# Kernel tuning notes

Hardware: AMD Instinct MI355X
Metric: run time of the kernel (lower is better)

## Reference

```python
import jax, jax.numpy as jnp
import numpy as np

M = 512          # n_clusters
D_PER = 32       # examples per cluster
FEAT = 1024      # embedding dim
ALPHA = 1.0
N_CLASSES = 128
EPS = 1e-8


def setup_inputs() -> dict:
    key = jax.random.key(0)
    k1, k2 = jax.random.split(key)
    N = M * D_PER
    inp = jax.random.normal(k1, (N, FEAT), dtype=jnp.float32)
    # class label per cluster, repeated d times so each contiguous chunk shares a class
    cluster_classes = jax.random.randint(k2, (M,), 0, N_CLASSES, dtype=jnp.int32)
    target = jnp.repeat(cluster_classes, D_PER)
    return {"input": inp, "target": target}


def reference(input, target):
    N, feat = input.shape
    m, d = M, D_PER
    # cluster assignment: sorted arange(m) repeated d times == repeat(arange(m), d)
    clusters = jnp.repeat(jnp.arange(m), d)                      # [N]
    cluster_classes = target[0 : m * d : d]                      # [m]

    # segment mean over contiguous equal-size chunks (== torch.chunk + mean + stack)
    means = input.reshape(m, d, feat).mean(axis=1)               # [m, feat]

    r2 = jnp.sum(input * input, axis=1, keepdims=True)           # [N,1]
    c2 = jnp.sum(means * means, axis=1)                          # [m]
    sample_costs = r2 + c2[None, :] - 2.0 * (input @ means.T)    # [N, m]

    # distance of each example to its own cluster mean
    intra = jnp.take_along_axis(sample_costs, clusters[:, None], axis=1)[:, 0]  # [N]

    variance = jnp.sum(intra) / float(N - 1)
    var_norm = -1.0 / (2.0 * variance ** 2)

    numerator = jnp.exp(var_norm * intra - ALPHA)                # [N]

    diff_class_mask = (target[:, None] != cluster_classes[None, :]).astype(input.dtype)  # [N,m]
    denominator = jnp.sum(diff_class_mask * jnp.exp(var_norm * sample_costs), axis=1)    # [N]

    losses = jax.nn.relu(-jnp.log(numerator / (denominator + EPS) + EPS))
    total_loss = jnp.mean(losses)

    pred = jnp.argmin(sample_costs, axis=1)                      # [N]
    acc = jnp.mean((pred == clusters).astype(jnp.float32))
    return total_loss, losses, pred, acc
```

## Files before the change

### kernel.cpp

```cpp
#include <hip/hip_runtime.h>
#include <math.h>

#define NCLUST 512
#define DPER 32
#define NFEAT 1024
#define NSAMP (NCLUST * DPER)
#define ALPHA_C 1.0f
#define EPS_C 1e-8f
#define MARGIN_C 0.25f

#define GBM 128
#define GBN 128
#define GBK 32
#define NCHUNK 8

typedef __attribute__((ext_vector_type(4))) float f32x4;
typedef __attribute__((ext_vector_type(8))) _Float16 f16x8;

__device__ __forceinline__ unsigned f2h(float f) {
  _Float16 h = (_Float16)f;
  return (unsigned)__builtin_bit_cast(ushort, h);
}

__device__ __forceinline__ void gload16(const ushort* g, ushort* l) {
  __builtin_amdgcn_global_load_lds(
      (const __attribute__((address_space(1))) unsigned int*)g,
      (__attribute__((address_space(3))) unsigned int*)l, 16, 0, 0);
}

__global__ __launch_bounds__(256) void k_pre(const float* __restrict__ inp,
                                             const int* __restrict__ target,
                                             float* __restrict__ means,
                                             ushort* __restrict__ Bf16,
                                             ushort* __restrict__ Af16,
                                             float* __restrict__ c2,
                                             float* __restrict__ r2g,
                                             float* __restrict__ intra,
                                             float* __restrict__ percl,
                                             int* __restrict__ ccls,
                                             int* __restrict__ wcount) {
  const int m = blockIdx.x;
  const int t = threadIdx.x;
  const int w = t >> 6, l = t & 63;
  __shared__ float ldsm[4][NFEAT];
  __shared__ float meanf[NFEAT];
  __shared__ float red4[4];
  __shared__ float redi[4];
  __shared__ float c2sh;

  const float* rowbase = inp + (size_t)m * DPER * NFEAT;
  ushort* arowbase = Af16 + (size_t)m * DPER * NFEAT;

  float4 macc0 = {0,0,0,0}, macc1 = {0,0,0,0}, macc2 = {0,0,0,0}, macc3 = {0,0,0,0};
  float r2keep[8];

  #pragma unroll 2
  for (int rr = 0; rr < 8; ++rr) {
    const int d = w * 8 + rr;
    const float* rp = rowbase + (size_t)d * NFEAT + l * 4;
    const float4 v0 = *(const float4*)(rp);
    const float4 v1 = *(const float4*)(rp + 256);
    const float4 v2 = *(const float4*)(rp + 512);
    const float4 v3 = *(const float4*)(rp + 768);
    ushort* ap = arowbase + (size_t)d * NFEAT + l * 4;
    uint2 h;
    h.x = f2h(v0.x) | (f2h(v0.y) << 16); h.y = f2h(v0.z) | (f2h(v0.w) << 16);
    *(uint2*)(ap) = h;
    h.x = f2h(v1.x) | (f2h(v1.y) << 16); h.y = f2h(v1.z) | (f2h(v1.w) << 16);
    *(uint2*)(ap + 256) = h;
    h.x = f2h(v2.x) | (f2h(v2.y) << 16); h.y = f2h(v2.z) | (f2h(v2.w) << 16);
    *(uint2*)(ap + 512) = h;
    h.x = f2h(v3.x) | (f2h(v3.y) << 16); h.y = f2h(v3.z) | (f2h(v3.w) << 16);
    *(uint2*)(ap + 768) = h;
    macc0.x += v0.x; macc0.y += v0.y; macc0.z += v0.z; macc0.w += v0.w;
    macc1.x += v1.x; macc1.y += v1.y; macc1.z += v1.z; macc1.w += v1.w;
    macc2.x += v2.x; macc2.y += v2.y; macc2.z += v2.z; macc2.w += v2.w;
    macc3.x += v3.x; macc3.y += v3.y; macc3.z += v3.z; macc3.w += v3.w;
    float p = v0.x*v0.x + v0.y*v0.y + v0.z*v0.z + v0.w*v0.w
            + v1.x*v1.x + v1.y*v1.y + v1.z*v1.z + v1.w*v1.w
            + v2.x*v2.x + v2.y*v2.y + v2.z*v2.z + v2.w*v2.w
            + v3.x*v3.x + v3.y*v3.y + v3.z*v3.z + v3.w*v3.w;
    #pragma unroll
    for (int off = 32; off; off >>= 1) p += __shfl_down(p, off);
    r2keep[rr] = p;
  }
  if (l == 0) {
    #pragma unroll
    for (int rr = 0; rr < 8; ++rr) r2g[m * DPER + w * 8 + rr] = r2keep[rr];
  }
  *(float4*)&ldsm[w][0 * 256 + l * 4] = macc0;
  *(float4*)&ldsm[w][1 * 256 + l * 4] = macc1;
  *(float4*)&ldsm[w][2 * 256 + l * 4] = macc2;
  *(float4*)&ldsm[w][3 * 256 + l * 4] = macc3;
  __syncthreads();
  float4 s0 = *(const float4*)&ldsm[0][t * 4];
  float4 s1 = *(const float4*)&ldsm[1][t * 4];
  float4 s2 = *(const float4*)&ldsm[2][t * 4];
  float4 s3 = *(const float4*)&ldsm[3][t * 4];
  const float inv = 1.0f / 32.0f;
  float4 mn;
  mn.x = (s0.x + s1.x + s2.x + s3.x) * inv;
  mn.y = (s0.y + s1.y + s2.y + s3.y) * inv;
  mn.z = (s0.z + s1.z + s2.z + s3.z) * inv;
  mn.w = (s0.w + s1.w + s2.w + s3.w) * inv;
  *(float4*)(means + (size_t)m * NFEAT + t * 4) = mn;
  uint2 bw;
  bw.x = f2h(mn.x) | (f2h(mn.y) << 16);
  bw.y = f2h(mn.z) | (f2h(mn.w) << 16);
  *(uint2*)&Bf16[(size_t)m * NFEAT + t * 4] = bw;
  *(float4*)&meanf[t * 4] = mn;
  float sq = mn.x * mn.x + mn.y * mn.y + mn.z * mn.z + mn.w * mn.w;
  #pragma unroll
  for (int off = 32; off; off >>= 1) sq += __shfl_down(sq, off);
  if (l == 0) red4[w] = sq;
  __syncthreads();
  if (t == 0) {
    const float cc = red4[0] + red4[1] + red4[2] + red4[3];
    c2sh = cc;
    c2[m] = cc;
    ccls[m] = target[m * DPER];
    if (m == 0) *wcount = 0;
  }
  __syncthreads();
  const float c2v = c2sh;
  float sintra = 0.f;
  #pragma unroll 2
  for (int rr = 0; rr < 8; ++rr) {
    const int d = w * 8 + rr;
    const float* rp = rowbase + (size_t)d * NFEAT + l * 4;
    const float4 v0 = *(const float4*)(rp);
    const float4 v1 = *(const float4*)(rp + 256);
    const float4 v2 = *(const float4*)(rp + 512);
    const float4 v3 = *(const float4*)(rp + 768);
    const float4 m0 = *(const float4*)&meanf[0 * 256 + l * 4];
    const float4 m1 = *(const float4*)&meanf[1 * 256 + l * 4];
    const float4 m2 = *(const float4*)&meanf[2 * 256 + l * 4];
    const float4 m3 = *(const float4*)&meanf[3 * 256 + l * 4];
    float p = v0.x*m0.x + v0.y*m0.y + v0.z*m0.z + v0.w*m0.w
            + v1.x*m1.x + v1.y*m1.y + v1.z*m1.z + v1.w*m1.w
            + v2.x*m2.x + v2.y*m2.y + v2.z*m2.z + v2.w*m2.w
            + v3.x*m3.x + v3.y*m3.y + v3.z*m3.z + v3.w*m3.w;
    #pragma unroll
    for (int off = 32; off; off >>= 1) p += __shfl_down(p, off);
    if (l == 0) {
      const float iv = r2keep[rr] + c2v - 2.0f * p;
      intra[m * DPER + d] = iv;
      sintra += iv;
    }
  }
  if (l == 0) redi[w] = sintra;
  __syncthreads();
  if (t == 0) percl[m] = redi[0] + redi[1] + redi[2] + redi[3];
}

__global__ __launch_bounds__(256, 2) void k_gemm(
    const ushort* __restrict__ Af16, const ushort* __restrict__ Bf16,
    const float* __restrict__ c2, const float* __restrict__ r2,
    const float* __restrict__ percl, const int* __restrict__ ccls,
    const int* __restrict__ target,
    float* __restrict__ den_p, float* __restrict__ minv_p,
    float* __restrict__ minv2_p, float* __restrict__ minc_p) {
  __shared__ ushort As[2][GBM * GBK];
  __shared__ ushort Bs[2][GBN * GBK];
  __shared__ float redv[4];
  const int t = threadIdx.x;
  const int l = t & 63, w = t >> 6;
  const int wg = (blockIdx.x & 7) * 64 + (blockIdx.x >> 3);
  const int rowblk = wg >> 2, colblk = wg & 3;
  const int row0 = rowblk * GBM, c0 = colblk * GBN;
  const int wr = w >> 1, wc = w & 1;

  const int sR = l >> 2;
  const int sg = (l & 3) ^ (sR & 3);
  const ushort* sA0 = Af16 + (size_t)(row0 + w * 32 + sR) * NFEAT + sg * 8;
  const ushort* sA1 = sA0 + 16 * NFEAT;
  const ushort* sB0 = Bf16 + (size_t)(c0 + w * 32 + sR) * NFEAT + sg * 8;
  const ushort* sB1 = sB0 + 16 * NFEAT;

  const int fr = l & 15, fq = l >> 4;
  const int ch = ((fq ^ (fr & 3)) * 8);

  f32x4 acc[4][4];
  #pragma unroll
  for (int i = 0; i < 4; ++i)
    #pragma unroll
    for (int j = 0; j < 4; ++j) acc[i][j] = (f32x4){0.f, 0.f, 0.f, 0.f};

#define STAGE(bi, ks) do {                                        \
    gload16(sA0 + (ks) * GBK, &As[bi][w * 32 * GBK]);             \
    gload16(sA1 + (ks) * GBK, &As[bi][w * 32 * GBK + 16 * GBK]);  \
    gload16(sB0 + (ks) * GBK, &Bs[bi][w * 32 * GBK]);             \
    gload16(sB1 + (ks) * GBK, &Bs[bi][w * 32 * GBK + 16 * GBK]);  \
  } while (0)

#define COMPUTE(bi) do {                                                     \
    f16x8 a[4], b[4];                                                        \
    _Pragma("unroll") for (int i = 0; i < 4; ++i)                            \
      a[i] = *(const f16x8*)&As[bi][(wr * 64 + i * 16 + fr) * GBK + ch];     \
    _Pragma("unroll") for (int j = 0; j < 4; ++j)                            \
      b[j] = *(const f16x8*)&Bs[bi][(wc * 64 + j * 16 + fr) * GBK + ch];     \
    _Pragma("unroll") for (int i = 0; i < 4; ++i)                            \
      _Pragma("unroll") for (int j = 0; j < 4; ++j)                          \
        acc[i][j] = __builtin_amdgcn_mfma_f32_16x16x32_f16(a[i], b[j],       \
                                                           acc[i][j], 0,0,0);\
  } while (0)

  STAGE(0, 0);
  #pragma unroll 1
  for (int ks = 0; ks < NFEAT / GBK - 2; ks += 2) {
    STAGE(1, ks + 1);
    asm volatile("s_waitcnt vmcnt(4)" ::: "memory");
    __builtin_amdgcn_s_barrier();
    COMPUTE(0);
    __builtin_amdgcn_s_barrier();
    STAGE(0, ks + 2);
    asm volatile("s_waitcnt vmcnt(4)" ::: "memory");
    __builtin_amdgcn_s_barrier();
    COMPUTE(1);
    __builtin_amdgcn_s_barrier();
  }
  STAGE(1, NFEAT / GBK - 1);
  asm volatile("s_waitcnt vmcnt(4)" ::: "memory");
  __builtin_amdgcn_s_barrier();
  COMPUTE(0);
  __builtin_amdgcn_s_barrier();
  asm volatile("s_waitcnt vmcnt(0)" ::: "memory");
  __builtin_amdgcn_s_barrier();
  COMPUTE(1);
#undef STAGE
#undef COMPUTE

  float vs = percl[t] + percl[t + 256];
  #pragma unroll
  for (int off = 32; off; off >>= 1) vs += __shfl_down(vs, off);
  if (l == 0) redv[w] = vs;
  __syncthreads();
  const float var = (redv[0] + redv[1] + redv[2] + redv[3]) / (float)(NSAMP - 1);
  const float vn = -1.0f / (2.0f * var * var);

  float c2j[4]; int clsj[4];
  #pragma unroll
  for (int j = 0; j < 4; ++j) {
    const int c = c0 + wc * 64 + j * 16 + fr;
    c2j[j] = c2[c];
    clsj[j] = ccls[c];
  }
  const int colchunk = colblk * 2 + wc;
  #pragma unroll
  for (int i = 0; i < 4; ++i) {
    const int rbase = row0 + wr * 64 + i * 16 + fq * 4;
    float r2v[4]; int tg[4];
    #pragma unroll
    for (int v = 0; v < 4; ++v) { r2v[v] = r2[rbase + v]; tg[v] = target[rbase + v]; }
    #pragma unroll
    for (int v = 0; v < 4; ++v) {
      float den = 0.f, bv = 3.4e38f, bv2 = 3.4e38f;
      int bc = 1 << 30;
      #pragma unroll
      for (int j = 0; j < 4; ++j) {
        const float cost = r2v[v] + c2j[j] - 2.0f * acc[i][j][v];
        if (clsj[j] != tg[v]) den += __expf(vn * cost);
        if (cost < bv) { bv2 = bv; bv = cost; bc = c0 + wc * 64 + j * 16 + fr; }
        else if (cost < bv2) { bv2 = cost; }
      }
      #pragma unroll
      for (int off = 1; off < 16; off <<= 1) {
        den += __shfl_xor(den, off);
        const float ov = __shfl_xor(bv, off);
        const float ov2 = __shfl_xor(bv2, off);
        const int oc = __shfl_xor(bc, off);
        const float nb2 = fminf(fminf(bv2, ov2), fmaxf(bv, ov));
        if (ov < bv || (ov == bv && oc < bc)) { bv = ov; bc = oc; }
        bv2 = nb2;
      }
      if (fr == 0) {
        const int idx = colchunk * NSAMP + rbase + v;
        den_p[idx] = den;
        minv_p[idx] = bv;
        minv2_p[idx] = bv2;
        minc_p[idx] = (float)bc;
      }
    }
  }
}

__global__ __launch_bounds__(256) void k_fin2(const float* __restrict__ den_p,
                                              const float* __restrict__ minv_p,
                                              const float* __restrict__ minv2_p,
                                              const float* __restrict__ minc_p,
                                              const float* __restrict__ intra,
                                              const float* __restrict__ percl,
                                              float* __restrict__ losses,
                                              int* __restrict__ wl,
                                              int* __restrict__ wcount,
                                              unsigned long long* __restrict__ slots) {
  __shared__ float redv[4];
  const int t = threadIdx.x;
  float vs = percl[t] + percl[t + 256];
  #pragma unroll
  for (int off = 32; off; off >>= 1) vs += __shfl_down(vs, off);
  if ((t & 63) == 0) redv[t >> 6] = vs;
  __syncthreads();
  const float var = (redv[0] + redv[1] + redv[2] + redv[3]) / (float)(NSAMP - 1);
  const float vn = -1.0f / (2.0f * var * var);

  const int row = blockIdx.x * 256 + t;
  float den = 0.f, bv = 3.4e38f, bv2 = 3.4e38f, bc = 0.f;
  #pragma unroll
  for (int k = 0; k < NCHUNK; ++k) {
    den += den_p[k * NSAMP + row];
    const float v = minv_p[k * NSAMP + row];
    const float v2 = minv2_p[k * NSAMP + row];
    const float c = minc_p[k * NSAMP + row];
    const float nb2 = fminf(fminf(bv2, v2), fmaxf(bv, v));
    if (v < bv) { bv = v; bc = c; }
    bv2 = nb2;
  }
  const float num = expf(vn * intra[row] - ALPHA_C);
  const float ratio = num / (den + EPS_C) + EPS_C;
  float loss = -logf(ratio);
  losses[row] = loss > 0.f ? loss : 0.f;
  if (bv2 - bv < MARGIN_C) {
    slots[row] = 0xFFFFFFFFFFFFFFFFULL;
    int i = atomicAdd(wcount, 1);
    wl[i] = row;
  } else {
    slots[row] = ((unsigned long long)__float_as_uint(bv) << 32) | (unsigned)(int)bc;
  }
}

__global__ __launch_bounds__(256) void k_fix(const float* __restrict__ inp,
                                             const float* __restrict__ means,
                                             const float* __restrict__ c2,
                                             const float* __restrict__ r2,
                                             const int* __restrict__ wl,
                                             const int* __restrict__ wcount,
                                             unsigned long long* __restrict__ slots) {
  __shared__ float rbuf[NFEAT];
  const int t = threadIdx.x;
  const int l = t & 63, w = t >> 6;
  const int cnt = *wcount;
  const int chunk = blockIdx.x & 63;
  for (int wi = blockIdx.x >> 6; wi < cnt; wi += gridDim.x >> 6) {
    const int row = wl[wi];
    __syncthreads();
    *(float4*)&rbuf[t * 4] = *(const float4*)(inp + (size_t)row * NFEAT + t * 4);
    __syncthreads();
    float rb[16];
    #pragma unroll
    for (int q = 0; q < 4; ++q) {
      const float4 v = *(const float4*)&rbuf[q * 256 + l * 4];
      rb[q * 4 + 0] = v.x; rb[q * 4 + 1] = v.y;
      rb[q * 4 + 2] = v.z; rb[q * 4 + 3] = v.w;
    }
    const float r2v = r2[row];
    #pragma unroll
    for (int cc = 0; cc < 2; ++cc) {
      const int c = chunk * 8 + w * 2 + cc;
      const float* mp = means + (size_t)c * NFEAT + l * 4;
      float dot = 0.f;
      #pragma unroll
      for (int q = 0; q < 4; ++q) {
        const float4 m4 = *(const float4*)(mp + q * 256);
        dot += m4.x * rb[q * 4 + 0] + m4.y * rb[q * 4 + 1] +
               m4.z * rb[q * 4 + 2] + m4.w * rb[q * 4 + 3];
      }
      #pragma unroll
      for (int off = 32; off; off >>= 1) dot += __shfl_down(dot, off);
      if (l == 0) {
        const float cost = r2v + c2[c] - 2.0f * dot;
        const unsigned long long enc =
            ((unsigned long long)__float_as_uint(cost) << 32) | (unsigned)c;
        atomicMin(&slots[row], enc);
      }
    }
  }
}

__global__ __launch_bounds__(256) void k_final(const float* __restrict__ losses,
                                               const unsigned long long* __restrict__ slots,
                                               float* __restrict__ preds,
                                               float* __restrict__ out) {
  const int t = threadIdx.x;
  float s = 0.f, cnt = 0.f;
  for (int i = t; i < NSAMP; i += 256) {
    s += losses[i];
    const int p = (int)(unsigned)(slots[i] & 0xFFFFFFFFULL);
    preds[i] = (float)p;
    cnt += (p == (i >> 5)) ? 1.f : 0.f;
  }
  __shared__ float redS[4], redC[4];
  #pragma unroll
  for (int off = 32; off > 0; off >>= 1) {
    s += __shfl_down(s, off);
    cnt += __shfl_down(cnt, off);
  }
  if ((t & 63) == 0) { redS[t >> 6] = s; redC[t >> 6] = cnt; }
  __syncthreads();
  if (t == 0) {
    out[0] = (redS[0] + redS[1] + redS[2] + redS[3]) / (float)NSAMP;
    out[1 + 2 * NSAMP] = (redC[0] + redC[1] + redC[2] + redC[3]) / (float)NSAMP;
  }
}

extern "C" void kernel_launch(void* const* d_in, const int* in_sizes, int n_in,
                              void* d_out, int out_size, void* d_ws, size_t ws_size,
                              hipStream_t stream) {
  const float* inp = (const float*)d_in[0];
  const int* target = (const int*)d_in[1];
  float* out = (float*)d_out;

  ushort* Af16 = (ushort*)d_ws;
  ushort* Bf16 = Af16 + (size_t)NSAMP * NFEAT;
  unsigned long long* slots =
      (unsigned long long*)(Bf16 + (size_t)NCLUST * NFEAT);
  float* means = (float*)(slots + NSAMP);
  float* c2 = means + (size_t)NCLUST * NFEAT;
  float* r2 = c2 + NCLUST;
  float* intra = r2 + NSAMP;
  float* vn = intra + NSAMP;
  float* percl = vn + 1;
  int* ccls = (int*)(percl + NCLUST);
  float* den_p = (float*)(ccls + NCLUST);
  float* minv_p = den_p + NCHUNK * NSAMP;
  float* minv2_p = minv_p + NCHUNK * NSAMP;
  float* minc_p = minv2_p + NCHUNK * NSAMP;
  int* wl = (int*)(minc_p + NCHUNK * NSAMP);
  int* wcount = wl + NSAMP;

  float* losses = out + 1;
  float* preds = out + 1 + NSAMP;

  hipLaunchKernelGGL(k_pre, dim3(NCLUST), dim3(256), 0, stream,
                     inp, target, means, Bf16, Af16, c2, r2, intra, percl, ccls, wcount);
  hipLaunchKernelGGL(k_gemm, dim3(512), dim3(256), 0, stream,
                     Af16, Bf16, c2, r2, percl, ccls, target,
                     den_p, minv_p, minv2_p, minc_p);
  hipLaunchKernelGGL(k_fin2, dim3(NSAMP / 256), dim3(256), 0, stream,
                     den_p, minv_p, minv2_p, minc_p, intra, percl, losses,
                     wl, wcount, slots);
  hipLaunchKernelGGL(k_fix, dim3(2048), dim3(256), 0, stream,
                     inp, means, c2, r2, wl, wcount, slots);
  hipLaunchKernelGGL(k_final, dim3(1), dim3(256), 0, stream,
                     losses, slots, preds, out);
}
```

Before: 98.09 us.

## Derive per-cluster intra sum algebraically and take intra distances from GEMM epilogue

```diff
diff --git a/kernel.cpp b/kernel.cpp
--- a/kernel.cpp
+++ b/kernel.cpp
@@ -35,7 +35,6 @@
                                              ushort* __restrict__ Af16,
                                              float* __restrict__ c2,
                                              float* __restrict__ r2g,
-                                             float* __restrict__ intra,
                                              float* __restrict__ percl,
                                              int* __restrict__ ccls,
                                              int* __restrict__ wcount) {
@@ -43,10 +42,8 @@
   const int t = threadIdx.x;
   const int w = t >> 6, l = t & 63;
   __shared__ float ldsm[4][NFEAT];
-  __shared__ float meanf[NFEAT];
   __shared__ float red4[4];
   __shared__ float redi[4];
-  __shared__ float c2sh;
 
   const float* rowbase = inp + (size_t)m * DPER * NFEAT;
   ushort* arowbase = Af16 + (size_t)m * DPER * NFEAT;
@@ -85,8 +82,13 @@
     r2keep[rr] = p;
   }
   if (l == 0) {
-    #pragma unroll
-    for (int rr = 0; rr < 8; ++rr) r2g[m * DPER + w * 8 + rr] = r2keep[rr];
+    float r2s = 0.f;
+    #pragma unroll
+    for (int rr = 0; rr < 8; ++rr) {
+      r2g[m * DPER + w * 8 + rr] = r2keep[rr];
+      r2s += r2keep[rr];
+    }
+    redi[w] = r2s;
   }
   *(float4*)&ldsm[w][0 * 256 + l * 4] = macc0;
   *(float4*)&ldsm[w][1 * 256 + l * 4] = macc1;
@@ -108,7 +110,6 @@
   bw.x = f2h(mn.x) | (f2h(mn.y) << 16);
   bw.y = f2h(mn.z) | (f2h(mn.w) << 16);
   *(uint2*)&Bf16[(size_t)m * NFEAT + t * 4] = bw;
-  *(float4*)&meanf[t * 4] = mn;
   float sq = mn.x * mn.x + mn.y * mn.y + mn.z * mn.z + mn.w * mn.w;
   #pragma unroll
   for (int off = 32; off; off >>= 1) sq += __shfl_down(sq, off);
@@ -116,41 +117,11 @@
   __syncthreads();
   if (t == 0) {
     const float cc = red4[0] + red4[1] + red4[2] + red4[3];
-    c2sh = cc;
     c2[m] = cc;
     ccls[m] = target[m * DPER];
+    percl[m] = (redi[0] + redi[1] + redi[2] + redi[3]) - 32.0f * cc;
     if (m == 0) *wcount = 0;
   }
-  __syncthreads();
-  const float c2v = c2sh;
-  float sintra = 0.f;
-  #pragma unroll 2
-  for (int rr = 0; rr < 8; ++rr) {
-    const int d = w * 8 + rr;
-    const float* rp = rowbase + (size_t)d * NFEAT + l * 4;
-    const float4 v0 = *(const float4*)(rp);
-    const float4 v1 = *(const float4*)(rp + 256);
-    const float4 v2 = *(const float4*)(rp + 512);
-    const float4 v3 = *(const float4*)(rp + 768);
-    const float4 m0 = *(const float4*)&meanf[0 * 256 + l * 4];
-    const float4 m1 = *(const float4*)&meanf[1 * 256 + l * 4];
-    const float4 m2 = *(const float4*)&meanf[2 * 256 + l * 4];
-    const float4 m3 = *(const float4*)&meanf[3 * 256 + l * 4];
-    float p = v0.x*m0.x + v0.y*m0.y + v0.z*m0.z + v0.w*m0.w
-            + v1.x*m1.x + v1.y*m1.y + v1.z*m1.z + v1.w*m1.w
-            + v2.x*m2.x + v2.y*m2.y + v2.z*m2.z + v2.w*m2.w
-            + v3.x*m3.x + v3.y*m3.y + v3.z*m3.z + v3.w*m3.w;
-    #pragma unroll
-    for (int off = 32; off; off >>= 1) p += __shfl_down(p, off);
-    if (l == 0) {
-      const float iv = r2keep[rr] + c2v - 2.0f * p;
-      intra[m * DPER + d] = iv;
-      sintra += iv;
-    }
-  }
-  if (l == 0) redi[w] = sintra;
-  __syncthreads();
-  if (t == 0) percl[m] = redi[0] + redi[1] + redi[2] + redi[3];
 }
 
 __global__ __launch_bounds__(256, 2) void k_gemm(
@@ -159,7 +130,8 @@
     const float* __restrict__ percl, const int* __restrict__ ccls,
     const int* __restrict__ target,
     float* __restrict__ den_p, float* __restrict__ minv_p,
-    float* __restrict__ minv2_p, float* __restrict__ minc_p) {
+    float* __restrict__ minv2_p, float* __restrict__ minc_p,
+    float* __restrict__ intra_g) {
   __shared__ ushort As[2][GBM * GBK];
   __shared__ ushort Bs[2][GBN * GBK];
   __shared__ float redv[4];
@@ -238,10 +210,11 @@
   const float var = (redv[0] + redv[1] + redv[2] + redv[3]) / (float)(NSAMP - 1);
   const float vn = -1.0f / (2.0f * var * var);
 
-  float c2j[4]; int clsj[4];
+  float c2j[4]; int clsj[4], cjv[4];
   #pragma unroll
   for (int j = 0; j < 4; ++j) {
     const int c = c0 + wc * 64 + j * 16 + fr;
+    cjv[j] = c;
     c2j[j] = c2[c];
     clsj[j] = ccls[c];
   }
@@ -249,6 +222,7 @@
   #pragma unroll
   for (int i = 0; i < 4; ++i) {
     const int rbase = row0 + wr * 64 + i * 16 + fq * 4;
+    const int cm = rbase >> 5;
     float r2v[4]; int tg[4];
     #pragma unroll
     for (int v = 0; v < 4; ++v) { r2v[v] = r2[rbase + v]; tg[v] = target[rbase + v]; }
@@ -260,7 +234,8 @@
       for (int j = 0; j < 4; ++j) {
         const float cost = r2v[v] + c2j[j] - 2.0f * acc[i][j][v];
         if (clsj[j] != tg[v]) den += __expf(vn * cost);
-        if (cost < bv) { bv2 = bv; bv = cost; bc = c0 + wc * 64 + j * 16 + fr; }
+        if (cjv[j] == cm) intra_g[rbase + v] = cost;
+        if (cost < bv) { bv2 = bv; bv = cost; bc = cjv[j]; }
         else if (cost < bv2) { bv2 = cost; }
       }
       #pragma unroll
@@ -288,7 +263,7 @@
                                               const float* __restrict__ minv_p,
                                               const float* __restrict__ minv2_p,
                                               const float* __restrict__ minc_p,
-                                              const float* __restrict__ intra,
+                                              const float* __restrict__ intra_g,
                                               const float* __restrict__ percl,
                                               float* __restrict__ losses,
                                               int* __restrict__ wl,
@@ -316,7 +291,7 @@
     if (v < bv) { bv = v; bc = c; }
     bv2 = nb2;
   }
-  const float num = expf(vn * intra[row] - ALPHA_C);
+  const float num = expf(vn * intra_g[row] - ALPHA_C);
   const float ratio = num / (den + EPS_C) + EPS_C;
   float loss = -logf(ratio);
   losses[row] = loss > 0.f ? loss : 0.f;
@@ -417,8 +392,8 @@
   float* means = (float*)(slots + NSAMP);
   float* c2 = means + (size_t)NCLUST * NFEAT;
   float* r2 = c2 + NCLUST;
-  float* intra = r2 + NSAMP;
-  float* vn = intra + NSAMP;
+  float* intra_g = r2 + NSAMP;
+  float* vn = intra_g + NSAMP;
   float* percl = vn + 1;
   int* ccls = (int*)(percl + NCLUST);
   float* den_p = (float*)(ccls + NCLUST);
@@ -432,12 +407,12 @@
   float* preds = out + 1 + NSAMP;
 
   hipLaunchKernelGGL(k_pre, dim3(NCLUST), dim3(256), 0, stream,
-                     inp, target, means, Bf16, Af16, c2, r2, intra, percl, ccls, wcount);
+                     inp, target, means, Bf16, Af16, c2, r2, percl, ccls, wcount);
   hipLaunchKernelGGL(k_gemm, dim3(512), dim3(256), 0, stream,
                      Af16, Bf16, c2, r2, percl, ccls, target,
-                     den_p, minv_p, minv2_p, minc_p);
+                     den_p, minv_p, minv2_p, minc_p, intra_g);
   hipLaunchKernelGGL(k_fin2, dim3(NSAMP / 256), dim3(256), 0, stream,
-                     den_p, minv_p, minv2_p, minc_p, intra, percl, losses,
+                     den_p, minv_p, minv2_p, minc_p, intra_g, percl, losses,
                      wl, wcount, slots);
   hipLaunchKernelGGL(k_fix, dim3(2048), dim3(256), 0, stream,
                      inp, means, c2, r2, wl, wcount, slots);
```

After: 88.67 us. -9.6%, faster.
